# Kernel tuning notes

Measured on AMD Instinct MI355X. Metric: run time of the kernel, lower is better.

The kernel has to match this reference:

```python
import jax, jax.numpy as jnp
import numpy as np

C = 128
HEADS = 4
GROUPS = 8
SHAPE = (1, C, 8, 24, 32)  # N, C, D, H, W
EPS = 1e-5


def setup_inputs() -> dict:
    key = jax.random.key(0)
    ks = jax.random.split(key, 3)
    x = jax.random.normal(ks[0], SHAPE, dtype=jnp.float32)
    mask = jnp.ones((1, 1) + SHAPE[2:], dtype=jnp.float32)
    qkv_w = jax.random.normal(ks[1], (3 * C, C), dtype=jnp.float32) * (1.0 / np.sqrt(C))
    qkv_b = jnp.zeros((3 * C,), dtype=jnp.float32)
    proj_w = jax.random.normal(ks[2], (C, C), dtype=jnp.float32) * (1.0 / np.sqrt(C))
    proj_b = jnp.zeros((C,), dtype=jnp.float32)
    return {
        'x': x, 'mask': mask,
        'gn_w': jnp.ones((C,), dtype=jnp.float32),
        'gn_b': jnp.zeros((C,), dtype=jnp.float32),
        'qkv_w': qkv_w, 'qkv_b': qkv_b,
        'proj_w': proj_w, 'proj_b': proj_b,
    }


def group_norm(x, w, b):
    N, Ch, D, H, W = x.shape
    xg = x.reshape(N, GROUPS, Ch // GROUPS, D, H, W)
    mu = jnp.mean(xg, axis=(2, 3, 4, 5), keepdims=True)
    var = jnp.var(xg, axis=(2, 3, 4, 5), keepdims=True)
    xg = (xg - mu) * jax.lax.rsqrt(var + EPS)
    x = xg.reshape(N, Ch, D, H, W)
    return x * w[None, :, None, None, None] + b[None, :, None, None, None]


def reference(x, mask, gn_w, gn_b, qkv_w, qkv_b, proj_w, proj_b):
    N, Ch, D, H, W = x.shape
    S = D * H * W
    hd = Ch // HEADS  # head dim
    xn = group_norm(x, gn_w, gn_b)
    # 1x1x1 conv == channel GEMM: [N,3C,S]
    qkv = jnp.einsum('ncs,oc->nos', xn.reshape(N, Ch, S), qkv_w) + qkv_b[None, :, None]
    q, k, v = jnp.split(qkv, 3, axis=1)
    # '(h c) s -> h s c' (head-major channel split)
    def to_heads(t):
        return t.reshape(N, HEADS, hd, S).transpose(0, 1, 3, 2)  # n h s c
    q, k, v = to_heads(q), to_heads(k), to_heads(v)
    scale = hd ** -0.5
    scores = jnp.einsum('nhic,nhjc->nhij', q, k) * scale
    probs = jax.nn.softmax(scores, axis=-1)
    out = jnp.einsum('nhij,nhjc->nhic', probs, v)
    # n h s c -> n (h c) s
    out = out.transpose(0, 1, 3, 2).reshape(N, Ch, S)
    out = jnp.einsum('ncs,oc->nos', out, proj_w) + proj_b[None, :, None]
    out = out.reshape(N, Ch, D, H, W)
    return (x + out) * mask, mask
```

## Files before the change

kernel.cpp:

```cpp
#include <hip/hip_runtime.h>
#include <hip/hip_bf16.h>
#include <cstddef>

typedef __bf16 bf16;
typedef __bf16 bf16x4 __attribute__((ext_vector_type(4)));
typedef __bf16 bf16x8 __attribute__((ext_vector_type(8)));
typedef float  f32x4  __attribute__((ext_vector_type(4)));

#define NC   128
#define NS   6144
#define HD   32
#define BKV  64
#define NSPLIT 4
#define NCH  ((NS / NSPLIT) / BKV)
#define GELEMS (16 * NS)
#define QK_SCALE (0.17677669529663689f * 1.4426950408889634f)

__device__ __forceinline__ f32x4 mfma16(bf16x8 a, bf16x8 b, f32x4 c) {
  return __builtin_amdgcn_mfma_f32_16x16x32_bf16(a, b, c, 0, 0, 0);
}
__device__ __forceinline__ void gl16(const bf16* g, void* s) {
  __builtin_amdgcn_global_load_lds((const __attribute__((address_space(1))) void*)g,
                                   (__attribute__((address_space(3))) void*)s, 16, 0, 0);
}
__device__ __forceinline__ int swz(int b) { return b ^ (((b >> 7) & 7) << 4); }

__global__ __launch_bounds__(256) void k_prep_stats(
    const float* __restrict__ qkv_w, const float* __restrict__ qkv_b,
    const float* __restrict__ proj_w, const float* __restrict__ x,
    bf16* __restrict__ wq, bf16* __restrict__ wp, float* __restrict__ bias_s,
    float* __restrict__ partials) {
  int bid = blockIdx.x;
  int tid = threadIdx.x;
  if (bid < 192) {
    int i = bid * 256 + tid;
    if (i < 3 * NC * NC) {
      float v = qkv_w[i];
      if (i < NC * NC) v *= QK_SCALE;
      wq[i] = (bf16)v;
    }
    if (i < NC * NC) wp[i] = (bf16)proj_w[i];
    if (i < 3 * NC) bias_s[i] = qkv_b[i] * ((i < NC) ? QK_SCALE : 1.0f);
    return;
  }
  int b = bid - 192;
  int g = b / 12, chunk = b % 12;
  float sum = 0.f, sq = 0.f;
  #pragma unroll
  for (int k = 0; k < 8; ++k) {
    int f4 = tid + k * 256;
    int c  = f4 >> 7;
    int s4 = f4 & 127;
    const float4 v = ((const float4*)x)[(size_t)(g * 16 + c) * (NS / 4) + chunk * 128 + s4];
    sum += v.x + v.y + v.z + v.w;
    sq  += v.x * v.x + v.y * v.y + v.z * v.z + v.w * v.w;
  }
  #pragma unroll
  for (int off = 32; off; off >>= 1) {
    sum += __shfl_down(sum, off, 64);
    sq  += __shfl_down(sq,  off, 64);
  }
  __shared__ float red[2][4];
  if ((tid & 63) == 0) { red[0][tid >> 6] = sum; red[1][tid >> 6] = sq; }
  __syncthreads();
  if (tid == 0) {
    partials[b * 2 + 0] = red[0][0] + red[0][1] + red[0][2] + red[0][3];
    partials[b * 2 + 1] = red[1][0] + red[1][1] + red[1][2] + red[1][3];
  }
}

__global__ __launch_bounds__(256) void k_qkv(
    const float* __restrict__ x, const float* __restrict__ partials,
    const float* __restrict__ gn_w, const float* __restrict__ gn_b,
    const bf16* __restrict__ wq, const float* __restrict__ bias_s,
    bf16* __restrict__ qg, bf16* __restrict__ kg, bf16* __restrict__ vtg) {
  int ot = blockIdx.x;
  int st = blockIdx.y;
  int tid = threadIdx.x;
  __shared__ __align__(16) char xn[64 * 256];
  __shared__ float swc[NC], sbc[NC];

  if (tid < NC) {
    int g = tid >> 4;
    float sum = 0.f, sq = 0.f;
    #pragma unroll
    for (int i = 0; i < 12; ++i) {
      sum += partials[(g * 12 + i) * 2 + 0];
      sq  += partials[(g * 12 + i) * 2 + 1];
    }
    float mean = sum * (1.0f / GELEMS);
    float var  = sq  * (1.0f / GELEMS) - mean * mean;
    float rstd = rsqrtf(var + 1e-5f);
    float wc = gn_w[tid] * rstd;
    swc[tid] = wc;
    sbc[tid] = gn_b[tid] - mean * wc;
  }
  __syncthreads();

  int s_local = tid & 63;
  int s_glob  = st * 64 + s_local;
  int wk = tid >> 6;
  #pragma unroll
  for (int i = 0; i < 4; ++i) {
    int c0 = (wk * 4 + i) * 8;
    bf16x8 ov;
    #pragma unroll
    for (int j = 0; j < 8; ++j) {
      int c = c0 + j;
      ov[j] = (bf16)(x[(size_t)c * NS + s_glob] * swc[c] + sbc[c]);
    }
    *(bf16x8*)(xn + ((s_local * 256 + c0 * 2) ^ ((s_local & 7) << 4))) = ov;
  }
  __syncthreads();

  int w = tid >> 6, l = tid & 63;
  int lr = l & 15, lg = l >> 4;
  int o_base = ot * 64 + (w >> 1) * 32;
  int sl_base = (w & 1) * 32;
  f32x4 acc[2][2] = {};
  #pragma unroll
  for (int k0 = 0; k0 < NC; k0 += 32) {
    bf16x8 a[2], b[2];
    #pragma unroll
    for (int m = 0; m < 2; ++m)
      a[m] = *(const bf16x8*)(wq + (size_t)(o_base + m * 16 + lr) * NC + k0 + lg * 8);
    #pragma unroll
    for (int n = 0; n < 2; ++n) {
      int row = sl_base + n * 16 + lr;
      b[n] = *(const bf16x8*)(xn + ((row * 256 + (k0 + lg * 8) * 2) ^ ((row & 7) << 4)));
    }
    #pragma unroll
    for (int m = 0; m < 2; ++m)
      #pragma unroll
      for (int n = 0; n < 2; ++n)
        acc[m][n] = mfma16(a[m], b[n], acc[m][n]);
  }
  #pragma unroll
  for (int m = 0; m < 2; ++m)
    #pragma unroll
    for (int n = 0; n < 2; ++n)
      #pragma unroll
      for (int r = 0; r < 4; ++r) {
        int o = o_base + m * 16 + lg * 4 + r;
        int s = st * 64 + sl_base + n * 16 + lr;
        float v = acc[m][n][r] + bias_s[o];
        int rem = o & 127, head = rem >> 5, c32 = rem & 31;
        if (o < NC)          qg[((size_t)head * NS + s) * HD + c32] = (bf16)v;
        else if (o < 2 * NC) kg[((size_t)head * NS + s) * HD + c32] = (bf16)v;
        else                 vtg[((size_t)head * HD + c32) * NS + s] = (bf16)v;
      }
}

__global__ __launch_bounds__(256, 6) void k_attn(
    const bf16* __restrict__ qg, const bf16* __restrict__ kg, const bf16* __restrict__ vtg,
    bf16* __restrict__ accP, float* __restrict__ ml) {
  const int h = blockIdx.y, sp = blockIdx.z;
  const int tid = threadIdx.x;
  const int w = tid >> 6, l = tid & 63;
  const int lr = l & 15, lg = l >> 4;
  const int qrow0 = blockIdx.x * 64 + w * 16;

  __shared__ __align__(16) char kbuf[2][4096];
  __shared__ __align__(16) char vbuf[2][4096];
  __shared__ __align__(16) char pbs[4][2048];
  char* pw = pbs[w];
  const int pswz  = (lr & 7) << 4;
  const int wbase = lr * 128 + lg * 8;
  const int rbase = lr * 128 + lg * 16;
  const int kswz  = ((lr >> 1) & 7) << 4;
  const int vswz  = (lr & 7) << 4;

  const bf16* qp = qg + (size_t)h * NS * HD;
  const bf16* kp = kg + (size_t)h * NS * HD;
  const bf16* vp = vtg + (size_t)h * HD * NS;

  bf16x8 qf = *(const bf16x8*)(qp + (size_t)(qrow0 + lr) * HD + lg * 8);

  bf16x8 ones;
  #pragma unroll
  for (int j = 0; j < 8; ++j) ones[j] = (bf16)1.0f;

  f32x4 acc0 = {}, acc1 = {};
  f32x4 lacc = {};
  const f32x4 zed = {};
  const int kv_beg = sp * (NS / NSPLIT);

  const int o_st = w * 1024 + (l << 4);
  const int u_st = swz(o_st);
  const bf16* ksrc = kp + (size_t)(kv_beg + (u_st >> 6)) * HD + ((u_st & 63) >> 1);
  const bf16* vsrc = vp + (size_t)(u_st >> 7) * NS + kv_beg + ((u_st & 127) >> 1);

  f32x4 sv[4];
  auto softmax_p = [&]() {
    #pragma unroll
    for (int t4 = 0; t4 < 4; ++t4) {
      #pragma unroll
      for (int r = 0; r < 4; ++r) sv[t4][r] = __builtin_amdgcn_exp2f(sv[t4][r]);
      bf16x4 pk;
      pk[0] = (bf16)sv[t4][0]; pk[1] = (bf16)sv[t4][1];
      pk[2] = (bf16)sv[t4][2]; pk[3] = (bf16)sv[t4][3];
      *(bf16x4*)(pw + ((wbase + t4 * 32) ^ pswz)) = pk;
    }
  };

  gl16(ksrc, kbuf[0] + w * 1024);
  gl16(vsrc, vbuf[0] + w * 1024);
  gl16(ksrc + BKV * HD, kbuf[1] + w * 1024);
  __syncthreads();
  #pragma unroll
  for (int t4 = 0; t4 < 4; ++t4) {
    bf16x8 kf = *(const bf16x8*)(kbuf[0] + (((t4 * 16 + lr) * 64 + lg * 16) ^ kswz));
    sv[t4] = mfma16(kf, qf, zed);
  }
  softmax_p();

  for (int t = 0; t < NCH; ++t) {
    const int cur = t & 1, nxt = cur ^ 1;
    const bool hn = (t + 1 < NCH);
    __syncthreads();
    if (hn) gl16(vsrc + (size_t)(t + 1) * BKV, vbuf[nxt] + w * 1024);
    if (t + 2 < NCH) gl16(ksrc + (size_t)(t + 2) * BKV * HD, kbuf[cur] + w * 1024);
    if (hn) {
      #pragma unroll
      for (int t4 = 0; t4 < 4; ++t4) {
        bf16x8 kf = *(const bf16x8*)(kbuf[nxt] + (((t4 * 16 + lr) * 64 + lg * 16) ^ kswz));
        sv[t4] = mfma16(kf, qf, zed);
      }
    }
    {
      const char* vb = vbuf[cur];
      bf16x8 pf0 = *(const bf16x8*)(pw + ((rbase + 0)  ^ pswz));
      bf16x8 pf1 = *(const bf16x8*)(pw + ((rbase + 64) ^ pswz));
      bf16x8 v00 = *(const bf16x8*)(vb + ((lr * 128 + 0  + lg * 16) ^ vswz));
      bf16x8 v10 = *(const bf16x8*)(vb + (((16 + lr) * 128 + 0  + lg * 16) ^ vswz));
      bf16x8 v01 = *(const bf16x8*)(vb + ((lr * 128 + 64 + lg * 16) ^ vswz));
      bf16x8 v11 = *(const bf16x8*)(vb + (((16 + lr) * 128 + 64 + lg * 16) ^ vswz));
      acc0 = mfma16(v00, pf0, acc0);
      acc1 = mfma16(v10, pf0, acc1);
      lacc = mfma16(ones, pf0, lacc);
      acc0 = mfma16(v01, pf1, acc0);
      acc1 = mfma16(v11, pf1, acc1);
      lacc = mfma16(ones, pf1, lacc);
    }
    if (hn) softmax_p();
  }

  bf16* base = accP + (size_t)(h * NSPLIT + sp) * 8 * NS * 4;
  size_t qrow = qrow0 + lr;
  bf16x4 o0, o1;
  #pragma unroll
  for (int r = 0; r < 4; ++r) { o0[r] = (bf16)acc0[r]; o1[r] = (bf16)acc1[r]; }
  *(bf16x4*)(base + ((size_t)lg * NS + qrow) * 4)       = o0;
  *(bf16x4*)(base + ((size_t)(4 + lg) * NS + qrow) * 4) = o1;
  if (lg == 0)
    ml[(size_t)(h * NSPLIT + sp) * NS + qrow] = lacc[0];
}

__global__ __launch_bounds__(256) void k_proj(
    const bf16* __restrict__ wp, const bf16* __restrict__ accP, const float* __restrict__ ml,
    const float* __restrict__ proj_b, const float* __restrict__ x,
    const float* __restrict__ mask, float* __restrict__ out) {
  int ot = blockIdx.x;
  int st = blockIdx.y;
  int tid = threadIdx.x;
  __shared__ __align__(16) char at[64 * 256];

  int s_local = tid & 63;
  int s = st * 64 + s_local;
  int wk = tid >> 6;
  if (ot == 0 && tid < 64)
    out[(size_t)NC * NS + st * 64 + tid] = mask[st * 64 + tid];
  #pragma unroll
  for (int i = 0; i < 4; ++i) {
    int c0 = (wk * 4 + i) * 8;
    int h = c0 >> 5;
    float L = 0.f;
    #pragma unroll
    for (int spl = 0; spl < NSPLIT; ++spl)
      L += ml[(size_t)(h * NSPLIT + spl) * NS + s];
    float inv = 1.0f / L;
    float o[8] = {};
    int cg0 = (c0 & 31) >> 2;
    #pragma unroll
    for (int spl = 0; spl < NSPLIT; ++spl) {
      const bf16* bp = accP + ((size_t)((h * NSPLIT + spl) * 8 + cg0) * NS + s) * 4;
      bf16x4 a0 = *(const bf16x4*)(bp);
      bf16x4 a1 = *(const bf16x4*)(bp + (size_t)NS * 4);
      #pragma unroll
      for (int j = 0; j < 4; ++j) {
        o[j]     += (float)a0[j];
        o[4 + j] += (float)a1[j];
      }
    }
    bf16x8 ov;
    #pragma unroll
    for (int j = 0; j < 8; ++j) ov[j] = (bf16)(o[j] * inv);
    *(bf16x8*)(at + ((s_local * 256 + c0 * 2) ^ ((s_local & 7) << 4))) = ov;
  }
  __syncthreads();

  int w = tid >> 6, l = tid & 63;
  int lr = l & 15, lg = l >> 4;
  int o_base = ot * 64 + (w >> 1) * 32;
  int sl_base = (w & 1) * 32;
  f32x4 acc[2][2] = {};
  #pragma unroll
  for (int k0 = 0; k0 < NC; k0 += 32) {
    bf16x8 a[2], b[2];
    #pragma unroll
    for (int m = 0; m < 2; ++m)
      a[m] = *(const bf16x8*)(wp + (size_t)(o_base + m * 16 + lr) * NC + k0 + lg * 8);
    #pragma unroll
    for (int n = 0; n < 2; ++n) {
      int row = sl_base + n * 16 + lr;
      b[n] = *(const bf16x8*)(at + ((row * 256 + (k0 + lg * 8) * 2) ^ ((row & 7) << 4)));
    }
    #pragma unroll
    for (int m = 0; m < 2; ++m)
      #pragma unroll
      for (int n = 0; n < 2; ++n)
        acc[m][n] = mfma16(a[m], b[n], acc[m][n]);
  }
  #pragma unroll
  for (int m = 0; m < 2; ++m)
    #pragma unroll
    for (int n = 0; n < 2; ++n)
      #pragma unroll
      for (int r = 0; r < 4; ++r) {
        int o = o_base + m * 16 + lg * 4 + r;
        int sg = st * 64 + sl_base + n * 16 + lr;
        float v = acc[m][n][r] + proj_b[o] + x[(size_t)o * NS + sg];
        out[(size_t)o * NS + sg] = v * mask[sg];
      }
}

extern "C" void kernel_launch(void* const* d_in, const int* in_sizes, int n_in,
                              void* d_out, int out_size, void* d_ws, size_t ws_size,
                              hipStream_t stream) {
  const float* x      = (const float*)d_in[0];
  const float* mask   = (const float*)d_in[1];
  const float* gn_w   = (const float*)d_in[2];
  const float* gn_b   = (const float*)d_in[3];
  const float* qkv_w  = (const float*)d_in[4];
  const float* qkv_b  = (const float*)d_in[5];
  const float* proj_w = (const float*)d_in[6];
  const float* proj_b = (const float*)d_in[7];

  char* ws = (char*)d_ws;
  float* partials = (float*)(ws + 0);
  float* bias_s   = (float*)(ws + 1024);
  bf16*  wq       = (bf16*)(ws + 4096);
  bf16*  wp       = (bf16*)(ws + 102400);
  bf16*  qg       = (bf16*)(ws + 135168);
  bf16*  kg       = (bf16*)(ws + 1708032);
  bf16*  vtg      = (bf16*)(ws + 3280896);
  bf16*  accP     = (bf16*)(ws + 4853760);
  float* ml       = (float*)(ws + 11145216);
  float* out      = (float*)d_out;

  k_prep_stats<<<288, 256, 0, stream>>>(qkv_w, qkv_b, proj_w, x, wq, wp, bias_s, partials);
  k_qkv       <<<dim3(6, 96), 256, 0, stream>>>(x, partials, gn_w, gn_b, wq, bias_s, qg, kg, vtg);
  k_attn      <<<dim3(96, 4, NSPLIT), 256, 0, stream>>>(qg, kg, vtg, accP, ml);
  k_proj      <<<dim3(2, 96), 256, 0, stream>>>(wp, accP, ml, proj_b, x, mask, out);
}
```

Before: 61.52 us.

## Keep softmax probabilities in registers instead of staging through LDS

The attention kernel now packs exp2 probabilities straight into MFMA B-operand fragments with v_cvt_pk_bf16_f32, which removes the per-wave LDS buffer and its write/read round trip. To make the register layout of P match the K-dimension ordering, V fragments are now assembled from two 8-byte LDS reads with a permuted k index. This cuts LDS traffic and shared memory per block, at the cost of more, narrower V loads and some register pressure.

```diff
diff --git a/kernel.cpp b/kernel.cpp
--- a/kernel.cpp
+++ b/kernel.cpp
@@ -24,6 +24,16 @@
                                    (__attribute__((address_space(3))) void*)s, 16, 0, 0);
 }
 __device__ __forceinline__ int swz(int b) { return b ^ (((b >> 7) & 7) << 4); }
+__device__ __forceinline__ unsigned cvtpk(float lo, float hi) {
+  unsigned r;
+  asm("v_cvt_pk_bf16_f32 %0, %1, %2" : "=v"(r) : "v"(lo), "v"(hi));
+  return r;
+}
+__device__ __forceinline__ bf16x8 mkfrag(unsigned a, unsigned b, unsigned c, unsigned d) {
+  union { unsigned u[4]; bf16x8 v; } t;
+  t.u[0] = a; t.u[1] = b; t.u[2] = c; t.u[3] = d;
+  return t.v;
+}
 
 __global__ __launch_bounds__(256) void k_prep_stats(
     const float* __restrict__ qkv_w, const float* __restrict__ qkv_b,
@@ -162,11 +172,6 @@
 
   __shared__ __align__(16) char kbuf[2][4096];
   __shared__ __align__(16) char vbuf[2][4096];
-  __shared__ __align__(16) char pbs[4][2048];
-  char* pw = pbs[w];
-  const int pswz  = (lr & 7) << 4;
-  const int wbase = lr * 128 + lg * 8;
-  const int rbase = lr * 128 + lg * 16;
   const int kswz  = ((lr >> 1) & 7) << 4;
   const int vswz  = (lr & 7) << 4;
 
@@ -191,16 +196,28 @@
   const bf16* vsrc = vp + (size_t)(u_st >> 7) * NS + kv_beg + ((u_st & 127) >> 1);
 
   f32x4 sv[4];
-  auto softmax_p = [&]() {
-    #pragma unroll
-    for (int t4 = 0; t4 < 4; ++t4) {
-      #pragma unroll
-      for (int r = 0; r < 4; ++r) sv[t4][r] = __builtin_amdgcn_exp2f(sv[t4][r]);
-      bf16x4 pk;
-      pk[0] = (bf16)sv[t4][0]; pk[1] = (bf16)sv[t4][1];
-      pk[2] = (bf16)sv[t4][2]; pk[3] = (bf16)sv[t4][3];
-      *(bf16x4*)(pw + ((wbase + t4 * 32) ^ pswz)) = pk;
-    }
+  bf16x8 pf0, pf1;
+
+  auto packP = [&]() {
+    float e0[4], e1[4], e2[4], e3[4];
+    #pragma unroll
+    for (int r = 0; r < 4; ++r) {
+      e0[r] = __builtin_amdgcn_exp2f(sv[0][r]);
+      e1[r] = __builtin_amdgcn_exp2f(sv[1][r]);
+      e2[r] = __builtin_amdgcn_exp2f(sv[2][r]);
+      e3[r] = __builtin_amdgcn_exp2f(sv[3][r]);
+    }
+    pf0 = mkfrag(cvtpk(e0[0], e0[1]), cvtpk(e0[2], e0[3]),
+                 cvtpk(e1[0], e1[1]), cvtpk(e1[2], e1[3]));
+    pf1 = mkfrag(cvtpk(e2[0], e2[1]), cvtpk(e2[2], e2[3]),
+                 cvtpk(e3[0], e3[1]), cvtpk(e3[2], e3[3]));
+  };
+  auto vfrag = [&](const char* vb, int row, int kk) -> bf16x8 {
+    int base = (row + lr) * 128 + kk * 64 + lg * 8;
+    union { bf16x4 h[2]; bf16x8 v; } u;
+    u.h[0] = *(const bf16x4*)(vb + ((base) ^ vswz));
+    u.h[1] = *(const bf16x4*)(vb + ((base + 32) ^ vswz));
+    return u.v;
   };
 
   gl16(ksrc, kbuf[0] + w * 1024);
@@ -212,7 +229,7 @@
     bf16x8 kf = *(const bf16x8*)(kbuf[0] + (((t4 * 16 + lr) * 64 + lg * 16) ^ kswz));
     sv[t4] = mfma16(kf, qf, zed);
   }
-  softmax_p();
+  packP();
 
   for (int t = 0; t < NCH; ++t) {
     const int cur = t & 1, nxt = cur ^ 1;
@@ -229,20 +246,14 @@
     }
     {
       const char* vb = vbuf[cur];
-      bf16x8 pf0 = *(const bf16x8*)(pw + ((rbase + 0)  ^ pswz));
-      bf16x8 pf1 = *(const bf16x8*)(pw + ((rbase + 64) ^ pswz));
-      bf16x8 v00 = *(const bf16x8*)(vb + ((lr * 128 + 0  + lg * 16) ^ vswz));
-      bf16x8 v10 = *(const bf16x8*)(vb + (((16 + lr) * 128 + 0  + lg * 16) ^ vswz));
-      bf16x8 v01 = *(const bf16x8*)(vb + ((lr * 128 + 64 + lg * 16) ^ vswz));
-      bf16x8 v11 = *(const bf16x8*)(vb + (((16 + lr) * 128 + 64 + lg * 16) ^ vswz));
-      acc0 = mfma16(v00, pf0, acc0);
-      acc1 = mfma16(v10, pf0, acc1);
+      acc0 = mfma16(vfrag(vb, 0,  0), pf0, acc0);
+      acc1 = mfma16(vfrag(vb, 16, 0), pf0, acc1);
       lacc = mfma16(ones, pf0, lacc);
-      acc0 = mfma16(v01, pf1, acc0);
-      acc1 = mfma16(v11, pf1, acc1);
+      acc0 = mfma16(vfrag(vb, 0,  1), pf1, acc0);
+      acc1 = mfma16(vfrag(vb, 16, 1), pf1, acc1);
       lacc = mfma16(ones, pf1, lacc);
     }
-    if (hn) softmax_p();
+    if (hn) packP();
   }
 
   bf16* base = accP + (size_t)(h * NSPLIT + sp) * 8 * NS * 4;
```

Result: faster. 58.43 us (-5.0%).
